# Kernel tuning notes

Measured on AMD Instinct MI355X. Metric: run time of the kernel, lower is better.

The kernel has to match this reference:

```python
import jax, jax.numpy as jnp
import numpy as np

N, E, B = 25000, 400000, 64          # nodes, edges, graphs
F, ED, H, C = 32, 8, 4, 32           # feature/edge dims, heads, per-head dim
HC = H * C
L = 4                                # init conv + 3 stacked convs (same shapes)
LIN = 128


def setup_inputs() -> dict:
    key = jax.random.key(0)
    ks = jax.random.split(key, 24)
    s = 0.05
    inp = {
        "x": jax.random.normal(ks[0], (N, F), jnp.float32),
        "edge_attr": jax.random.normal(ks[1], (E, ED), jnp.float32),
        "edge_index": jax.random.randint(ks[2], (2, E), 0, N),
        "batch_index": jnp.sort(jax.random.randint(ks[3], (N,), 0, B)),
        # stacked TransformerConv params (leading dim = layer)
        "Wq": jax.random.normal(ks[4], (L, F, HC), jnp.float32) * s,
        "bq": jnp.zeros((L, HC), jnp.float32),
        "Wk": jax.random.normal(ks[5], (L, F, HC), jnp.float32) * s,
        "bk": jnp.zeros((L, HC), jnp.float32),
        "Wv": jax.random.normal(ks[6], (L, F, HC), jnp.float32) * s,
        "bv": jnp.zeros((L, HC), jnp.float32),
        "We": jax.random.normal(ks[7], (L, ED, HC), jnp.float32) * s,
        "be": jnp.zeros((L, HC), jnp.float32),
        "Wskip": jax.random.normal(ks[8], (L, F, HC), jnp.float32) * s,
        "bskip": jnp.zeros((L, HC), jnp.float32),
        "Wbeta": jax.random.normal(ks[9], (L, 3 * HC, 1), jnp.float32) * s,
        # per-layer Linear(H*C -> emb) + BatchNorm
        "Wlin": jax.random.normal(ks[10], (L, HC, F), jnp.float32) * s,
        "blin": jnp.zeros((L, F), jnp.float32),
        "bn_gamma": jnp.ones((L, F), jnp.float32),
        "bn_beta": jnp.zeros((L, F), jnp.float32),
        # readout MLP
        "W1": jax.random.normal(ks[11], (2 * F, LIN), jnp.float32) * s,
        "b1": jnp.zeros((LIN,), jnp.float32),
        "W2": jax.random.normal(ks[12], (LIN, LIN // 2), jnp.float32) * s,
        "b2": jnp.zeros((LIN // 2,), jnp.float32),
        "W3": jax.random.normal(ks[13], (LIN // 2, 1), jnp.float32) * s,
        "b3": jnp.zeros((1,), jnp.float32),
    }
    return inp


def _transformer_conv(x, edge_attr, src, dst, Wq, bq, Wk, bk, Wv, bv, We, be,
                      Wskip, bskip, Wbeta):
    """PyG TransformerConv(heads=H, concat=True, beta=True, edge_dim=ED), eval mode."""
    n = x.shape[0]
    q = (x @ Wq + bq).reshape(n, H, C)
    k = (x @ Wk + bk).reshape(n, H, C)
    v = (x @ Wv + bv).reshape(n, H, C)
    e = (edge_attr @ We + be).reshape(-1, H, C)          # [E,H,C]
    kj = k[src] + e                                       # key_j + edge
    alpha = jnp.einsum('ehc,ehc->eh', q[dst], kj) / np.sqrt(C).astype(np.float32)
    # segment softmax over incoming edges per destination node
    amax = jax.ops.segment_max(alpha, dst, num_segments=n)
    a = jnp.exp(alpha - amax[dst])
    denom = jax.ops.segment_sum(a, dst, num_segments=n)
    a = a / denom[dst]                                    # [E,H]
    msg = (v[src] + e) * a[:, :, None]
    out = jax.ops.segment_sum(msg, dst, num_segments=n).reshape(n, HC)
    x_skip = x @ Wskip + bskip
    beta = jax.nn.sigmoid(
        jnp.concatenate([out, x_skip, out - x_skip], axis=-1) @ Wbeta)  # [N,1]
    return beta * x_skip + (1.0 - beta) * out


def _bn(h, gamma, beta):
    m = h.mean(axis=0)
    v = h.var(axis=0)
    return (h - m) * jax.lax.rsqrt(v + 1e-5) * gamma + beta


def reference(x, edge_attr, edge_index, batch_index,
              Wq, bq, Wk, bk, Wv, bv, We, be, Wskip, bskip, Wbeta,
              Wlin, blin, bn_gamma, bn_beta, W1, b1, W2, b2, W3, b3):
    src, dst = edge_index[0], edge_index[1]
    counts = jax.ops.segment_sum(jnp.ones((N,), jnp.float32), batch_index,
                                 num_segments=B)[:, None]
    h = x
    rep = jnp.zeros((B, 2 * F), jnp.float32)
    for i in range(L):
        h = _transformer_conv(h, edge_attr, src, dst,
                              Wq[i], bq[i], Wk[i], bk[i], Wv[i], bv[i],
                              We[i], be[i], Wskip[i], bskip[i], Wbeta[i])
        h = jax.nn.elu(h @ Wlin[i] + blin[i])
        h = _bn(h, bn_gamma[i], bn_beta[i])
        if i > 0:  # original pools only inside the n_layers loop
            gmx = jax.ops.segment_max(h, batch_index, num_segments=B)
            gmean = jax.ops.segment_sum(h, batch_index, num_segments=B) / counts
            rep = rep + jnp.concatenate([gmx, gmean], axis=1)
    z = jax.nn.elu(rep @ W1 + b1)
    z = jax.nn.elu(z @ W2 + b2)
    return z @ W3 + b3  # [B,1]
```

## Files before the change

kernel.cpp:

```cpp
#include <hip/hip_runtime.h>
#include <hip/hip_bf16.h>
#include <hip/hip_fp16.h>
#include <math.h>

#define NN 25000
#define EE 400000
#define BB 64
#define FF 32
#define EDD 8
#define HH 4
#define CC 32
#define HCC 128
#define LL 4
#define LINN 128

#define RSQRT_C 0.17677669529663687f
#define NREP 16
#define NREPP 8
#define GMAX_OFF (NREP * 64)
#define GSUM_OFF (NREP * 64 + NREPP * BB * 32)
#define LSTATS_WORDS (NREP * 64 + 2 * NREPP * BB * 32)


__global__ void deg_kernel(const int* __restrict__ dst, int* __restrict__ deg) {
    int i = blockIdx.x * blockDim.x + threadIdx.x;
    if (i < EE) atomicAdd(&deg[dst[i]], 1);
}

__global__ void scan1_kernel(const int* __restrict__ deg, int* __restrict__ rowp, int* __restrict__ blks) {
    __shared__ int s[256];
    int i = blockIdx.x * 256 + threadIdx.x;
    int v = (i < NN) ? deg[i] : 0;
    s[threadIdx.x] = v;
    __syncthreads();
    for (int off = 1; off < 256; off <<= 1) {
        int t = (threadIdx.x >= off) ? s[threadIdx.x - off] : 0;
        __syncthreads();
        s[threadIdx.x] += t;
        __syncthreads();
    }
    if (i < NN) rowp[i + 1] = s[threadIdx.x];
    if (threadIdx.x == 255) blks[blockIdx.x] = s[255];
    if (i == 0) rowp[0] = 0;
}

__global__ void scan2_kernel(int* __restrict__ blks, int nb,
                             const int* __restrict__ bidx, int* __restrict__ gstart) {
    __shared__ int s[128];
    int t = threadIdx.x;
    int v = (t < nb) ? blks[t] : 0;
    s[t] = v;
    __syncthreads();
    for (int off = 1; off < 128; off <<= 1) {
        int u = (t >= off) ? s[t - off] : 0;
        __syncthreads();
        s[t] += u;
        __syncthreads();
    }
    if (t < nb) blks[t] = s[t] - v;
    if (t <= BB) {
        int lo = 0, hi = NN;
        while (lo < hi) { int mid = (lo + hi) >> 1; if (bidx[mid] < t) lo = mid + 1; else hi = mid; }
        gstart[t] = lo;
    }
}

__global__ void scan3_kernel(int* __restrict__ rowp, const int* __restrict__ blks) {
    int i = blockIdx.x * 256 + threadIdx.x;
    if (i < NN) rowp[i + 1] += blks[blockIdx.x];
}

__global__ void fill_kernel(const int* __restrict__ dst, const int* __restrict__ rowp,
                            int* __restrict__ cnt2, int* __restrict__ eid) {
    int i = blockIdx.x * blockDim.x + threadIdx.x;
    if (i < EE) {
        int d = dst[i];
        int pos = rowp[d] + atomicAdd(&cnt2[d], 1);
        eid[pos] = i;
    }
}

__global__ void sortseg_kernel(const int* __restrict__ rowp, int* __restrict__ eid) {
    int n = blockIdx.x * 256 + threadIdx.x;
    if (n >= NN) return;
    int b = rowp[n], e = rowp[n + 1];
    int d = e - b;
    if (d <= 1) return;
    if (d <= 64) {
        int buf[64];
        for (int i = 0; i < d; ++i) buf[i] = eid[b + i];
        for (int i = 1; i < d; ++i) {
            int key = buf[i];
            int j = i - 1;
            while (j >= 0 && buf[j] > key) { buf[j + 1] = buf[j]; --j; }
            buf[j + 1] = key;
        }
        for (int i = 0; i < d; ++i) eid[b + i] = buf[i];
    } else {
        for (int i = b + 1; i < e; ++i) {
            int key = eid[i];
            int j = i - 1;
            while (j >= b && eid[j] > key) { eid[j + 1] = eid[j]; --j; }
            eid[j + 1] = key;
        }
    }
}

__global__ void csr_gather_kernel(const int* __restrict__ csre, const int* __restrict__ srcA,
                                  const float* __restrict__ eattr,
                                  int* __restrict__ csrsrc, uint4* __restrict__ eh) {
    int j = blockIdx.x * blockDim.x + threadIdx.x;
    if (j < EE) {
        int e = csre[j];
        csrsrc[j] = srcA[e];
        const float4* s = (const float4*)(eattr + (size_t)e * 8);
        float4 s0 = s[0], s1 = s[1];
        __half2 h0 = __float22half2_rn(make_float2(s0.x, s0.y));
        __half2 h1 = __float22half2_rn(make_float2(s0.z, s0.w));
        __half2 h2 = __float22half2_rn(make_float2(s1.x, s1.y));
        __half2 h3 = __float22half2_rn(make_float2(s1.z, s1.w));
        uint4 o;
        o.x = *(unsigned*)&h0; o.y = *(unsigned*)&h1;
        o.z = *(unsigned*)&h2; o.w = *(unsigned*)&h3;
        eh[j] = o;
    }
}

__global__ __launch_bounds__(256) void qkvs_kernel(
    const float* __restrict__ hin, int applyBN,
    const float* __restrict__ lstats_prev, float* __restrict__ lstats_cur,
    const float* __restrict__ gamma, const float* __restrict__ bnbeta,
    const float* __restrict__ Wq, const float* __restrict__ bq,
    const float* __restrict__ Wk, const float* __restrict__ bk,
    const float* __restrict__ Wv, const float* __restrict__ bv,
    const float* __restrict__ Ws, const float* __restrict__ bs,
    __half2* __restrict__ qo, __half2* __restrict__ kvo,
    __half2* __restrict__ so)
{
    if (blockIdx.x == 0) {
        for (int i = threadIdx.x; i < LSTATS_WORDS; i += 256) lstats_cur[i] = 0.0f;
    }
    __shared__ float xs[32][32];
    __shared__ float sbns[64];
    if (threadIdx.x < 32) {
        float scale = 1.0f, shift = 0.0f;
        if (applyBN) {
            float sm = 0.0f, sq = 0.0f;
#pragma unroll
            for (int r = 0; r < NREP; ++r) {
                sm += lstats_prev[r * 64 + threadIdx.x];
                sq += lstats_prev[r * 64 + 32 + threadIdx.x];
            }
            float mean = sm * (1.0f / NN);
            float var = sq * (1.0f / NN) - mean * mean;
            scale = gamma[threadIdx.x] * rsqrtf(var + 1e-5f);
            shift = bnbeta[threadIdx.x] - mean * scale;
        }
        sbns[threadIdx.x] = scale;
        sbns[32 + threadIdx.x] = shift;
    }
    int lane = threadIdx.x & 63;
    int sel = threadIdx.x >> 6;
    const float* W = (sel == 0) ? Wq : (sel == 1) ? Wk : (sel == 2) ? Wv : Ws;
    const float* bias = (sel == 0) ? bq : (sel == 1) ? bk : (sel == 2) ? bv : bs;
    float w0[32], w1[32];
#pragma unroll
    for (int f = 0; f < 32; ++f) {
        float2 t = *(const float2*)&W[f * 128 + 2 * lane];
        w0[f] = t.x; w1[f] = t.y;
    }
    float2 bvv = *(const float2*)&bias[2 * lane];

    int c = lane >> 1;
    int pr = lane & 1;
    int h2k = c * 4 + pr;
    int h2v = c * 4 + 2 + pr;

    for (int chunk = blockIdx.x * 32; chunk < NN; chunk += gridDim.x * 32) {
        __syncthreads();
        for (int i = threadIdx.x; i < 1024; i += 256) {
            int nn = chunk + (i >> 5);
            int ch = i & 31;
            float v = (nn < NN) ? hin[nn * 32 + ch] : 0.0f;
            xs[i >> 5][ch] = v * sbns[ch] + sbns[32 + ch];
        }
        __syncthreads();
        int nmax = NN - chunk; if (nmax > 32) nmax = 32;
        for (int nl = 0; nl < nmax; ++nl) {
            float a0 = bvv.x, a1 = bvv.y;
#pragma unroll
            for (int f4 = 0; f4 < 8; ++f4) {
                float4 xv = *(const float4*)&xs[nl][f4 * 4];
                a0 = fmaf(xv.x, w0[f4 * 4],     a0);
                a1 = fmaf(xv.x, w1[f4 * 4],     a1);
                a0 = fmaf(xv.y, w0[f4 * 4 + 1], a0);
                a1 = fmaf(xv.y, w1[f4 * 4 + 1], a1);
                a0 = fmaf(xv.z, w0[f4 * 4 + 2], a0);
                a1 = fmaf(xv.z, w1[f4 * 4 + 2], a1);
                a0 = fmaf(xv.w, w0[f4 * 4 + 3], a0);
                a1 = fmaf(xv.w, w1[f4 * 4 + 3], a1);
            }
            size_t node = (size_t)(chunk + nl);
            __half2 hv = __float22half2_rn(make_float2(a0, a1));
            if (sel == 0)      qo[node * 64 + lane] = hv;
            else if (sel == 1) kvo[node * 128 + h2k] = hv;
            else if (sel == 2) kvo[node * 128 + h2v] = hv;
            else               so[node * 64 + lane] = hv;
        }
    }
}

__device__ __forceinline__ unsigned fmap_u(float x) {
    unsigned u = __float_as_uint(x);
    return (u & 0x80000000u) ? ~u : (u | 0x80000000u);
}
__device__ __forceinline__ float funmap_u(unsigned u) {
    unsigned b = (u & 0x80000000u) ? (u & 0x7fffffffu) : ~u;
    return __uint_as_float(b);
}

__global__ __launch_bounds__(256) void attn_kernel(
    const uint2* __restrict__ qh, const uint4* __restrict__ kvb4,
    const uint2* __restrict__ skh,
    const uint4* __restrict__ eh,
    const int* __restrict__ srcArr,
    const int* __restrict__ rowp,
    const int* __restrict__ bidx,
    const float* __restrict__ WeL, const float* __restrict__ beL,
    const float* __restrict__ WbL,
    const float* __restrict__ WlinL, const float* __restrict__ blinL,
    float* __restrict__ hlin, float* __restrict__ lstats,
    int doPool, int doWriteH)
{
    __shared__ __align__(16) float shc[4 * 128];
    __shared__ float sbn[64];

    int tid = threadIdx.x;
    if (tid < 64) sbn[tid] = 0.0f;
    __syncthreads();

    int w = tid >> 6;
    int lane = tid & 63;
    int n = blockIdx.x * 4 + w;

    if (n < NN) {
        int c = lane & 31;
        int h = lane >> 5;

        float4 we[8];
#pragma unroll
        for (int d = 0; d < 8; ++d) we[d] = *(const float4*)&WeL[d * 128 + 4 * c];
        float4 be4 = *(const float4*)&beL[4 * c];

        uint2 qraw = qh[(size_t)n * 32 + c];
        float2 q01 = __half22float2(*(const __half2*)&qraw.x);
        float2 q23 = __half22float2(*(const __half2*)&qraw.y);
        float4 q4 = make_float4(q01.x * RSQRT_C, q01.y * RSQRT_C,
                                q23.x * RSQRT_C, q23.y * RSQRT_C);

        int beg = rowp[n], end = rowp[n + 1];
        int cnt = end - beg;
        int last = end - 1;

        float s = 0.0f, a0 = 0.0f, a1 = 0.0f, a2 = 0.0f, a3 = 0.0f;

        uint4 kvA = make_uint4(0u, 0u, 0u, 0u), kvB = kvA;
        uint4 eaA = kvA, eaB = kvA;
        int snC = 0, snD = 0;

        if (cnt > 0) {
            int j0 = beg + h;     j0 = (j0 < end) ? j0 : last;
            int j1 = beg + 2 + h; j1 = (j1 < end) ? j1 : last;
            int j2 = beg + 4 + h; j2 = (j2 < end) ? j2 : last;
            int j3 = beg + 6 + h; j3 = (j3 < end) ? j3 : last;
            int snA = srcArr[j0];
            int snB = srcArr[j1];
            snC = srcArr[j2];
            snD = srcArr[j3];
            kvA = kvb4[(size_t)snA * 32 + c];
            kvB = kvb4[(size_t)snB * 32 + c];
            eaA = eh[j0];
            eaB = eh[j1];
        }

        for (int jb = beg; jb < end; jb += 2) {
            int j = jb + h;
            uint4 kvC = kvb4[(size_t)snC * 32 + c];
            int jn = (j + 4 < end) ? j + 4 : last;
            uint4 eaC = eh[jn];
            int j8 = (j + 8 < end) ? j + 8 : last;
            int snE = srcArr[j8];

            float2 e01 = __half22float2(*(const __half2*)&eaA.x);
            float2 e23 = __half22float2(*(const __half2*)&eaA.y);
            float2 e45 = __half22float2(*(const __half2*)&eaA.z);
            float2 e67 = __half22float2(*(const __half2*)&eaA.w);
            float ead[8] = { e01.x, e01.y, e23.x, e23.y, e45.x, e45.y, e67.x, e67.y };

            float ex = be4.x, ey = be4.y, ez = be4.z, ew = be4.w;
#pragma unroll
            for (int d = 0; d < 8; ++d) {
                ex = fmaf(ead[d], we[d].x, ex);
                ey = fmaf(ead[d], we[d].y, ey);
                ez = fmaf(ead[d], we[d].z, ez);
                ew = fmaf(ead[d], we[d].w, ew);
            }

            float2 k01 = __half22float2(*(const __half2*)&kvA.x);
            float2 k23 = __half22float2(*(const __half2*)&kvA.y);
            float2 v01 = __half22float2(*(const __half2*)&kvA.z);
            float2 v23 = __half22float2(*(const __half2*)&kvA.w);

            float p = q4.x * (k01.x + ex) + q4.y * (k01.y + ey)
                    + q4.z * (k23.x + ez) + q4.w * (k23.y + ew);
            p += __shfl_xor(p, 1);
            p += __shfl_xor(p, 2);
            p += __shfl_xor(p, 4);
            float wg = (j < end) ? __expf(p) : 0.0f;
            s += wg;
            a0 = fmaf(wg, v01.x + ex, a0);
            a1 = fmaf(wg, v01.y + ey, a1);
            a2 = fmaf(wg, v23.x + ez, a2);
            a3 = fmaf(wg, v23.y + ew, a3);

            kvA = kvB; kvB = kvC;
            eaA = eaB; eaB = eaC;
            snC = snD; snD = snE;
        }

        s  += __shfl_xor(s, 32);
        a0 += __shfl_xor(a0, 32);
        a1 += __shfl_xor(a1, 32);
        a2 += __shfl_xor(a2, 32);
        a3 += __shfl_xor(a3, 32);

        float rs = (cnt > 0) ? (1.0f / s) : 0.0f;
        float o0 = a0 * rs, o1 = a1 * rs, o2 = a2 * rs, o3 = a3 * rs;

        uint2 skraw = skh[(size_t)n * 32 + c];
        float2 s01 = __half22float2(*(const __half2*)&skraw.x);
        float2 s23 = __half22float2(*(const __half2*)&skraw.y);
        float4 sk4 = make_float4(s01.x, s01.y, s23.x, s23.y);

        float4 wbo = *(const float4*)&WbL[4 * c];
        float4 wbs = *(const float4*)&WbL[128 + 4 * c];
        float4 wbd = *(const float4*)&WbL[256 + 4 * c];

        float t = o0 * wbo.x + sk4.x * wbs.x + (o0 - sk4.x) * wbd.x
                + o1 * wbo.y + sk4.y * wbs.y + (o1 - sk4.y) * wbd.y
                + o2 * wbo.z + sk4.z * wbs.z + (o2 - sk4.z) * wbd.z
                + o3 * wbo.w + sk4.w * wbs.w + (o3 - sk4.w) * wbd.w;
#pragma unroll
        for (int off = 1; off <= 16; off <<= 1) t += __shfl_xor(t, off);
        float beta = 1.0f / (1.0f + __expf(-t));
        float4 hc4;
        hc4.x = beta * sk4.x + (1.0f - beta) * o0;
        hc4.y = beta * sk4.y + (1.0f - beta) * o1;
        hc4.z = beta * sk4.z + (1.0f - beta) * o2;
        hc4.w = beta * sk4.w + (1.0f - beta) * o3;
        if (h == 0) ((float4*)shc)[w * 32 + c] = hc4;
        int cc = lane & 31;
        int half = lane >> 5;
        float acc = 0.0f;
#pragma unroll 8
        for (int i = 0; i < 64; ++i) {
            int ch = half * 64 + i;
            acc += shc[w * 128 + ch] * WlinL[ch * 32 + cc];
        }
        acc += __shfl_xor(acc, 32);
        if (lane < 32) {
            float hv = acc + blinL[lane];
            hv = (hv > 0.0f) ? hv : expm1f(hv);
            if (doWriteH) hlin[n * 32 + lane] = hv;
            atomicAdd(&sbn[lane], hv);
            atomicAdd(&sbn[32 + lane], hv * hv);
            if (doPool) {
                int g = bidx[n];
                int repv = blockIdx.x & (NREPP - 1);
                size_t idx = ((size_t)repv * BB + g) * 32 + lane;
                atomicMax((unsigned*)lstats + GMAX_OFF + idx, fmap_u(hv));
                atomicAdd(lstats + GSUM_OFF + idx, hv);
            }
        }
    }
    __syncthreads();
    if (tid < 64) atomicAdd(&lstats[(blockIdx.x & (NREP - 1)) * 64 + tid], sbn[tid]);
}

__global__ void repupd_kernel(const float* __restrict__ lstats,
                              const float* __restrict__ gamma, const float* __restrict__ bnbeta,
                              const int* __restrict__ gstart, float* __restrict__ rep, int assign) {
    int i = blockIdx.x * blockDim.x + threadIdx.x;
    if (i < BB * 32) {
        int g = i >> 5, ch = i & 31;
        float sm = 0.0f, sq = 0.0f;
#pragma unroll
        for (int r = 0; r < NREP; ++r) { sm += lstats[r * 64 + ch]; sq += lstats[r * 64 + 32 + ch]; }
        float mean = sm * (1.0f / NN);
        float var = sq * (1.0f / NN) - mean * mean;
        float scale = gamma[ch] * rsqrtf(var + 1e-5f);
        float shift = bnbeta[ch] - mean * scale;

        int cntg = gstart[g + 1] - gstart[g];
        float vmax = 0.0f, vmean = 0.0f;
        if (cntg > 0) {
            const unsigned* gm = (const unsigned*)lstats + GMAX_OFF;
            const float* gs = lstats + GSUM_OFF;
            unsigned mx = 0u;
            float sum = 0.0f;
#pragma unroll
            for (int r = 0; r < NREPP; ++r) {
                size_t idx = ((size_t)r * BB + g) * 32 + ch;
                unsigned m = gm[idx];
                mx = (m > mx) ? m : mx;
                sum += gs[idx];
            }
            vmax = scale * funmap_u(mx) + shift;
            vmean = scale * (sum / (float)cntg) + shift;
        }
        if (assign) {
            rep[g * 64 + ch] = vmax;
            rep[g * 64 + 32 + ch] = vmean;
        } else {
            rep[g * 64 + ch] += vmax;
            rep[g * 64 + 32 + ch] += vmean;
        }
    }
}

__device__ __forceinline__ float eluf(float x) { return x > 0.0f ? x : expm1f(x); }

__global__ __launch_bounds__(128) void readout_kernel(
    const float* __restrict__ rep,
    const float* __restrict__ W1, const float* __restrict__ b1,
    const float* __restrict__ W2, const float* __restrict__ b2,
    const float* __restrict__ W3, const float* __restrict__ b3,
    float* __restrict__ out)
{
    __shared__ float sr[64];
    __shared__ float sz1[128];
    __shared__ float sz2[64];
    int g = blockIdx.x;
    int t = threadIdx.x;
    if (t < 64) sr[t] = rep[g * 64 + t];
    __syncthreads();
    float acc = b1[t];
#pragma unroll 8
    for (int i = 0; i < 64; ++i) acc += sr[i] * W1[i * 128 + t];
    sz1[t] = eluf(acc);
    __syncthreads();
    if (t < 64) {
        float a2 = b2[t];
#pragma unroll 8
        for (int i = 0; i < 128; ++i) a2 += sz1[i] * W2[i * 64 + t];
        sz2[t] = eluf(a2);
    }
    __syncthreads();
    if (t < 64) {
        float p = sz2[t] * W3[t];
#pragma unroll
        for (int off = 1; off <= 32; off <<= 1) p += __shfl_xor(p, off);
        if (t == 0) out[g] = p + b3[0];
    }
}


extern "C" void kernel_launch(void* const* d_in, const int* in_sizes, int n_in,
                              void* d_out, int out_size, void* d_ws, size_t ws_size,
                              hipStream_t stream) {
    const float* x      = (const float*)d_in[0];
    const float* eattr  = (const float*)d_in[1];
    const int*   eidx   = (const int*)d_in[2];
    const int*   bidx   = (const int*)d_in[3];
    const float* Wq     = (const float*)d_in[4];
    const float* bq     = (const float*)d_in[5];
    const float* Wk     = (const float*)d_in[6];
    const float* bk     = (const float*)d_in[7];
    const float* Wv     = (const float*)d_in[8];
    const float* bv     = (const float*)d_in[9];
    const float* We     = (const float*)d_in[10];
    const float* be     = (const float*)d_in[11];
    const float* Wskip  = (const float*)d_in[12];
    const float* bskip  = (const float*)d_in[13];
    const float* Wbeta  = (const float*)d_in[14];
    const float* Wlin   = (const float*)d_in[15];
    const float* blin   = (const float*)d_in[16];
    const float* bng    = (const float*)d_in[17];
    const float* bnb    = (const float*)d_in[18];
    const float* W1     = (const float*)d_in[19];
    const float* b1     = (const float*)d_in[20];
    const float* W2     = (const float*)d_in[21];
    const float* b2     = (const float*)d_in[22];
    const float* W3     = (const float*)d_in[23];
    const float* b3     = (const float*)d_in[24];
    float* out = (float*)d_out;

    char* ws = (char*)d_ws;
    size_t off = 0;
    auto alloc = [&](size_t bytes) -> char* {
        char* p = ws + off;
        off = (off + bytes + 255) & ~(size_t)255;
        return p;
    };
    int*     rowp   = (int*)alloc((NN + 1) * 4);
    int*     degcnt = (int*)alloc(2 * NN * 4);
    int*     deg    = degcnt;
    int*     cnt2   = degcnt + NN;
    int*     csre   = (int*)alloc(EE * 4);
    int*     blks   = (int*)alloc(128 * 4);
    int*     gstart = (int*)alloc((BB + 1) * 4);
    float*   rep    = (float*)alloc(BB * 64 * 4);
    __half2* qH     = (__half2*)alloc((size_t)NN * 64 * 4);
    __half2* kvB    = (__half2*)alloc((size_t)NN * 128 * 4);
    __half2* skH    = (__half2*)alloc((size_t)NN * 64 * 4);
    float*   hlin   = (float*)alloc((size_t)NN * 32 * 4);
    float*   lstats = (float*)alloc(2 * LSTATS_WORDS * 4);
    int*     csrsrc = (int*)alloc(EE * 4);
    uint4*   ecsrh  = (uint4*)alloc((size_t)EE * 16);

    const int* srcA = eidx;
    const int* dstA = eidx + EE;

    (void)hipMemsetAsync(degcnt, 0, 2 * NN * 4, stream);

    deg_kernel<<<(EE + 255) / 256, 256, 0, stream>>>(dstA, deg);
    scan1_kernel<<<98, 256, 0, stream>>>(deg, rowp, blks);
    scan2_kernel<<<1, 128, 0, stream>>>(blks, 98, bidx, gstart);
    scan3_kernel<<<98, 256, 0, stream>>>(rowp, blks);
    fill_kernel<<<(EE + 255) / 256, 256, 0, stream>>>(dstA, rowp, cnt2, csre);
    sortseg_kernel<<<98, 256, 0, stream>>>(rowp, csre);
    csr_gather_kernel<<<(EE + 255) / 256, 256, 0, stream>>>(csre, srcA, eattr, csrsrc, ecsrh);

    for (int l = 0; l < LL; ++l) {
        float* lcur = lstats + (size_t)(l & 1) * LSTATS_WORDS;
        float* lprev = lstats + (size_t)((l & 1) ^ 1) * LSTATS_WORDS;

        qkvs_kernel<<<782, 256, 0, stream>>>(
            (l == 0) ? x : hlin, (l > 0) ? 1 : 0,
            lprev, lcur,
            bng + (l > 0 ? (l - 1) : 0) * FF, bnb + (l > 0 ? (l - 1) : 0) * FF,
            Wq + l * FF * HCC, bq + l * HCC,
            Wk + l * FF * HCC, bk + l * HCC,
            Wv + l * FF * HCC, bv + l * HCC,
            Wskip + l * FF * HCC, bskip + l * HCC,
            qH, kvB, skH);

        attn_kernel<<<(NN + 3) / 4, 256, 0, stream>>>(
            (const uint2*)qH, (const uint4*)kvB, (const uint2*)skH,
            ecsrh, csrsrc, rowp, bidx,
            We + l * EDD * HCC, be + l * HCC,
            Wbeta + l * 3 * HCC,
            Wlin + l * HCC * FF, blin + l * FF,
            hlin, lcur,
            (l > 0) ? 1 : 0, (l < LL - 1) ? 1 : 0);

        if (l > 0) {
            repupd_kernel<<<8, 256, 0, stream>>>(lcur, bng + l * FF, bnb + l * FF,
                                                 gstart, rep, (l == 1) ? 1 : 0);
        }
    }

    readout_kernel<<<64, 128, 0, stream>>>(rep, W1, b1, W2, b2, W3, b3, out);
}
```

Measured before the change: 532.3 us.

## Schedule attention nodes by descending degree and fold pooling update into readout

```diff
diff --git a/kernel.cpp b/kernel.cpp
--- a/kernel.cpp
+++ b/kernel.cpp
@@ -27,11 +27,13 @@
     if (i < EE) atomicAdd(&deg[dst[i]], 1);
 }
 
-__global__ void scan1_kernel(const int* __restrict__ deg, int* __restrict__ rowp, int* __restrict__ blks) {
+__global__ void scan1_kernel(const int* __restrict__ deg, int* __restrict__ rowp,
+                             int* __restrict__ blks, int* __restrict__ hist) {
     __shared__ int s[256];
     int i = blockIdx.x * 256 + threadIdx.x;
     int v = (i < NN) ? deg[i] : 0;
     s[threadIdx.x] = v;
+    if (i < NN) atomicAdd(&hist[v < 255 ? v : 255], 1);
     __syncthreads();
     for (int off = 1; off < 256; off <<= 1) {
         int t = (threadIdx.x >= off) ? s[threadIdx.x - off] : 0;
@@ -44,8 +46,27 @@
     if (i == 0) rowp[0] = 0;
 }
 
-__global__ void scan2_kernel(int* __restrict__ blks, int nb,
-                             const int* __restrict__ bidx, int* __restrict__ gstart) {
+__global__ void scan2_kernel(const int* __restrict__ bidx, int* __restrict__ gstart,
+                             const int* __restrict__ hist, int* __restrict__ binstart) {
+    __shared__ int sb[256];
+    int t = threadIdx.x;
+    sb[t] = hist[t];
+    __syncthreads();
+    for (int off = 1; off < 256; off <<= 1) {
+        int u = (t + off < 256) ? sb[t + off] : 0;
+        __syncthreads();
+        sb[t] += u;
+        __syncthreads();
+    }
+    binstart[t] = sb[t] - hist[t];
+    if (t <= BB) {
+        int lo = 0, hi = NN;
+        while (lo < hi) { int mid = (lo + hi) >> 1; if (bidx[mid] < t) lo = mid + 1; else hi = mid; }
+        gstart[t] = lo;
+    }
+}
+
+__global__ void scan2b_kernel(int* __restrict__ blks, int nb) {
     __shared__ int s[128];
     int t = threadIdx.x;
     int v = (t < nb) ? blks[t] : 0;
@@ -58,16 +79,18 @@
         __syncthreads();
     }
     if (t < nb) blks[t] = s[t] - v;
-    if (t <= BB) {
-        int lo = 0, hi = NN;
-        while (lo < hi) { int mid = (lo + hi) >> 1; if (bidx[mid] < t) lo = mid + 1; else hi = mid; }
-        gstart[t] = lo;
-    }
-}
-
-__global__ void scan3_kernel(int* __restrict__ rowp, const int* __restrict__ blks) {
+}
+
+__global__ void scan3_kernel(int* __restrict__ rowp, const int* __restrict__ blks,
+                             const int* __restrict__ deg, const int* __restrict__ binstart,
+                             int* __restrict__ bincnt, int* __restrict__ perm) {
     int i = blockIdx.x * 256 + threadIdx.x;
-    if (i < NN) rowp[i + 1] += blks[blockIdx.x];
+    if (i < NN) {
+        rowp[i + 1] += blks[blockIdx.x];
+        int d = deg[i]; d = (d < 255) ? d : 255;
+        int pos = binstart[d] + atomicAdd(&bincnt[d], 1);
+        perm[pos] = i;
+    }
 }
 
 __global__ void fill_kernel(const int* __restrict__ dst, const int* __restrict__ rowp,
@@ -226,6 +249,7 @@
     const int* __restrict__ srcArr,
     const int* __restrict__ rowp,
     const int* __restrict__ bidx,
+    const int* __restrict__ perm,
     const float* __restrict__ WeL, const float* __restrict__ beL,
     const float* __restrict__ WbL,
     const float* __restrict__ WlinL, const float* __restrict__ blinL,
@@ -234,16 +258,18 @@
 {
     __shared__ __align__(16) float shc[4 * 128];
     __shared__ float sbn[64];
+    __shared__ int snode[4];
 
     int tid = threadIdx.x;
     if (tid < 64) sbn[tid] = 0.0f;
+    if (tid < 4) snode[tid] = perm[blockIdx.x * 4 + tid];
     __syncthreads();
 
     int w = tid >> 6;
     int lane = tid & 63;
-    int n = blockIdx.x * 4 + w;
-
-    if (n < NN) {
+    int n = snode[w];
+
+    {
         int c = lane & 31;
         int h = lane >> 5;
 
@@ -387,51 +413,11 @@
     if (tid < 64) atomicAdd(&lstats[(blockIdx.x & (NREP - 1)) * 64 + tid], sbn[tid]);
 }
 
-__global__ void repupd_kernel(const float* __restrict__ lstats,
-                              const float* __restrict__ gamma, const float* __restrict__ bnbeta,
-                              const int* __restrict__ gstart, float* __restrict__ rep, int assign) {
-    int i = blockIdx.x * blockDim.x + threadIdx.x;
-    if (i < BB * 32) {
-        int g = i >> 5, ch = i & 31;
-        float sm = 0.0f, sq = 0.0f;
-#pragma unroll
-        for (int r = 0; r < NREP; ++r) { sm += lstats[r * 64 + ch]; sq += lstats[r * 64 + 32 + ch]; }
-        float mean = sm * (1.0f / NN);
-        float var = sq * (1.0f / NN) - mean * mean;
-        float scale = gamma[ch] * rsqrtf(var + 1e-5f);
-        float shift = bnbeta[ch] - mean * scale;
-
-        int cntg = gstart[g + 1] - gstart[g];
-        float vmax = 0.0f, vmean = 0.0f;
-        if (cntg > 0) {
-            const unsigned* gm = (const unsigned*)lstats + GMAX_OFF;
-            const float* gs = lstats + GSUM_OFF;
-            unsigned mx = 0u;
-            float sum = 0.0f;
-#pragma unroll
-            for (int r = 0; r < NREPP; ++r) {
-                size_t idx = ((size_t)r * BB + g) * 32 + ch;
-                unsigned m = gm[idx];
-                mx = (m > mx) ? m : mx;
-                sum += gs[idx];
-            }
-            vmax = scale * funmap_u(mx) + shift;
-            vmean = scale * (sum / (float)cntg) + shift;
-        }
-        if (assign) {
-            rep[g * 64 + ch] = vmax;
-            rep[g * 64 + 32 + ch] = vmean;
-        } else {
-            rep[g * 64 + ch] += vmax;
-            rep[g * 64 + 32 + ch] += vmean;
-        }
-    }
-}
-
 __device__ __forceinline__ float eluf(float x) { return x > 0.0f ? x : expm1f(x); }
 
 __global__ __launch_bounds__(128) void readout_kernel(
-    const float* __restrict__ rep,
+    const float* __restrict__ lstats, const int* __restrict__ gstart,
+    const float* __restrict__ bng, const float* __restrict__ bnb,
     const float* __restrict__ W1, const float* __restrict__ b1,
     const float* __restrict__ W2, const float* __restrict__ b2,
     const float* __restrict__ W3, const float* __restrict__ b3,
@@ -440,9 +426,41 @@
     __shared__ float sr[64];
     __shared__ float sz1[128];
     __shared__ float sz2[64];
+    __shared__ float sss[64];
     int g = blockIdx.x;
     int t = threadIdx.x;
-    if (t < 64) sr[t] = rep[g * 64 + t];
+    if (t < 64) sr[t] = 0.0f;
+    int cntg = gstart[g + 1] - gstart[g];
+    for (int l = 1; l < LL; ++l) {
+        const float* lst = lstats + (size_t)l * LSTATS_WORDS;
+        __syncthreads();
+        if (t < 32) {
+            float sm = 0.0f, sq = 0.0f;
+#pragma unroll
+            for (int r = 0; r < NREP; ++r) { sm += lst[r * 64 + t]; sq += lst[r * 64 + 32 + t]; }
+            float mean = sm * (1.0f / NN);
+            float var = sq * (1.0f / NN) - mean * mean;
+            float scale = bng[l * FF + t] * rsqrtf(var + 1e-5f);
+            sss[t] = scale;
+            sss[32 + t] = bnb[l * FF + t] - mean * scale;
+        }
+        __syncthreads();
+        if (t < 32 && cntg > 0) {
+            const unsigned* gm = (const unsigned*)lst + GMAX_OFF;
+            const float* gs = lst + GSUM_OFF;
+            unsigned mx = 0u;
+            float sum = 0.0f;
+#pragma unroll
+            for (int r = 0; r < NREPP; ++r) {
+                size_t idx = ((size_t)r * BB + g) * 32 + t;
+                unsigned m = gm[idx];
+                mx = (m > mx) ? m : mx;
+                sum += gs[idx];
+            }
+            sr[t]      += sss[t] * funmap_u(mx) + sss[32 + t];
+            sr[32 + t] += sss[t] * (sum / (float)cntg) + sss[32 + t];
+        }
+    }
     __syncthreads();
     float acc = b1[t];
 #pragma unroll 8
@@ -503,37 +521,41 @@
         return p;
     };
     int*     rowp   = (int*)alloc((NN + 1) * 4);
-    int*     degcnt = (int*)alloc(2 * NN * 4);
-    int*     deg    = degcnt;
-    int*     cnt2   = degcnt + NN;
+    int*     zeroed = (int*)alloc((2 * NN + 512) * 4);
+    int*     deg    = zeroed;
+    int*     cnt2   = zeroed + NN;
+    int*     hist   = zeroed + 2 * NN;
+    int*     bincnt = zeroed + 2 * NN + 256;
+    int*     binstart = (int*)alloc(256 * 4);
+    int*     perm   = (int*)alloc(NN * 4);
     int*     csre   = (int*)alloc(EE * 4);
     int*     blks   = (int*)alloc(128 * 4);
     int*     gstart = (int*)alloc((BB + 1) * 4);
-    float*   rep    = (float*)alloc(BB * 64 * 4);
     __half2* qH     = (__half2*)alloc((size_t)NN * 64 * 4);
     __half2* kvB    = (__half2*)alloc((size_t)NN * 128 * 4);
     __half2* skH    = (__half2*)alloc((size_t)NN * 64 * 4);
     float*   hlin   = (float*)alloc((size_t)NN * 32 * 4);
-    float*   lstats = (float*)alloc(2 * LSTATS_WORDS * 4);
+    float*   lstats = (float*)alloc((size_t)LL * LSTATS_WORDS * 4);
     int*     csrsrc = (int*)alloc(EE * 4);
     uint4*   ecsrh  = (uint4*)alloc((size_t)EE * 16);
 
     const int* srcA = eidx;
     const int* dstA = eidx + EE;
 
-    (void)hipMemsetAsync(degcnt, 0, 2 * NN * 4, stream);
+    (void)hipMemsetAsync(zeroed, 0, (2 * NN + 512) * 4, stream);
 
     deg_kernel<<<(EE + 255) / 256, 256, 0, stream>>>(dstA, deg);
-    scan1_kernel<<<98, 256, 0, stream>>>(deg, rowp, blks);
-    scan2_kernel<<<1, 128, 0, stream>>>(blks, 98, bidx, gstart);
-    scan3_kernel<<<98, 256, 0, stream>>>(rowp, blks);
+    scan1_kernel<<<98, 256, 0, stream>>>(deg, rowp, blks, hist);
+    scan2_kernel<<<1, 256, 0, stream>>>(bidx, gstart, hist, binstart);
+    scan2b_kernel<<<1, 128, 0, stream>>>(blks, 98);
+    scan3_kernel<<<98, 256, 0, stream>>>(rowp, blks, deg, binstart, bincnt, perm);
     fill_kernel<<<(EE + 255) / 256, 256, 0, stream>>>(dstA, rowp, cnt2, csre);
     sortseg_kernel<<<98, 256, 0, stream>>>(rowp, csre);
     csr_gather_kernel<<<(EE + 255) / 256, 256, 0, stream>>>(csre, srcA, eattr, csrsrc, ecsrh);
 
     for (int l = 0; l < LL; ++l) {
-        float* lcur = lstats + (size_t)(l & 1) * LSTATS_WORDS;
-        float* lprev = lstats + (size_t)((l & 1) ^ 1) * LSTATS_WORDS;
+        float* lcur = lstats + (size_t)l * LSTATS_WORDS;
+        float* lprev = lstats + (size_t)(l > 0 ? l - 1 : 0) * LSTATS_WORDS;
 
         qkvs_kernel<<<782, 256, 0, stream>>>(
             (l == 0) ? x : hlin, (l > 0) ? 1 : 0,
@@ -547,18 +569,14 @@
 
         attn_kernel<<<(NN + 3) / 4, 256, 0, stream>>>(
             (const uint2*)qH, (const uint4*)kvB, (const uint2*)skH,
-            ecsrh, csrsrc, rowp, bidx,
+            ecsrh, csrsrc, rowp, bidx, perm,
             We + l * EDD * HCC, be + l * HCC,
             Wbeta + l * 3 * HCC,
             Wlin + l * HCC * FF, blin + l * FF,
             hlin, lcur,
             (l > 0) ? 1 : 0, (l < LL - 1) ? 1 : 0);
-
-        if (l > 0) {
-            repupd_kernel<<<8, 256, 0, stream>>>(lcur, bng + l * FF, bnb + l * FF,
-                                                 gstart, rep, (l == 1) ? 1 : 0);
-        }
-    }
-
-    readout_kernel<<<64, 128, 0, stream>>>(rep, W1, b1, W2, b2, W3, b3, out);
-}
+    }
+
+    readout_kernel<<<64, 128, 0, stream>>>(lstats, gstart, bng, bnb,
+                                           W1, b1, W2, b2, W3, b3, out);
+}
```

Result: slower. 616.3 us (+15.8%).

## Order attention nodes by in-degree bins to balance warps per block

Applied to the files above, without the earlier changes.

```diff
diff --git a/kernel.cpp b/kernel.cpp
--- a/kernel.cpp
+++ b/kernel.cpp
@@ -27,11 +27,13 @@
     if (i < EE) atomicAdd(&deg[dst[i]], 1);
 }
 
-__global__ void scan1_kernel(const int* __restrict__ deg, int* __restrict__ rowp, int* __restrict__ blks) {
+__global__ void scan1_kernel(const int* __restrict__ deg, int* __restrict__ rowp,
+                             int* __restrict__ blks, int* __restrict__ hist) {
     __shared__ int s[256];
     int i = blockIdx.x * 256 + threadIdx.x;
     int v = (i < NN) ? deg[i] : 0;
     s[threadIdx.x] = v;
+    if (i < NN) atomicAdd(&hist[v < 255 ? v : 255], 1);
     __syncthreads();
     for (int off = 1; off < 256; off <<= 1) {
         int t = (threadIdx.x >= off) ? s[threadIdx.x - off] : 0;
@@ -65,9 +67,30 @@
     }
 }
 
-__global__ void scan3_kernel(int* __restrict__ rowp, const int* __restrict__ blks) {
+__global__ void binprep_kernel(const int* __restrict__ hist, int* __restrict__ binstart) {
+    __shared__ int sb[256];
+    int t = threadIdx.x;
+    sb[t] = hist[t];
+    __syncthreads();
+    for (int off = 1; off < 256; off <<= 1) {
+        int u = (t + off < 256) ? sb[t + off] : 0;
+        __syncthreads();
+        sb[t] += u;
+        __syncthreads();
+    }
+    binstart[t] = sb[t] - hist[t];
+}
+
+__global__ void scan3_kernel(int* __restrict__ rowp, const int* __restrict__ blks,
+                             const int* __restrict__ deg, const int* __restrict__ binstart,
+                             int* __restrict__ bincnt, int* __restrict__ perm) {
     int i = blockIdx.x * 256 + threadIdx.x;
-    if (i < NN) rowp[i + 1] += blks[blockIdx.x];
+    if (i < NN) {
+        rowp[i + 1] += blks[blockIdx.x];
+        int d = deg[i]; d = (d < 255) ? d : 255;
+        int pos = binstart[d] + atomicAdd(&bincnt[d], 1);
+        perm[pos] = i;
+    }
 }
 
 __global__ void fill_kernel(const int* __restrict__ dst, const int* __restrict__ rowp,
@@ -226,6 +249,7 @@
     const int* __restrict__ srcArr,
     const int* __restrict__ rowp,
     const int* __restrict__ bidx,
+    const int* __restrict__ perm,
     const float* __restrict__ WeL, const float* __restrict__ beL,
     const float* __restrict__ WbL,
     const float* __restrict__ WlinL, const float* __restrict__ blinL,
@@ -234,16 +258,18 @@
 {
     __shared__ __align__(16) float shc[4 * 128];
     __shared__ float sbn[64];
+    __shared__ int snode[4];
 
     int tid = threadIdx.x;
     if (tid < 64) sbn[tid] = 0.0f;
+    if (tid < 4) snode[tid] = perm[blockIdx.x * 4 + tid];
     __syncthreads();
 
     int w = tid >> 6;
     int lane = tid & 63;
-    int n = blockIdx.x * 4 + w;
-
-    if (n < NN) {
+    int n = snode[w];
+
+    {
         int c = lane & 31;
         int h = lane >> 5;
 
@@ -503,9 +529,13 @@
         return p;
     };
     int*     rowp   = (int*)alloc((NN + 1) * 4);
-    int*     degcnt = (int*)alloc(2 * NN * 4);
-    int*     deg    = degcnt;
-    int*     cnt2   = degcnt + NN;
+    int*     zeroed = (int*)alloc((2 * NN + 512) * 4);
+    int*     deg    = zeroed;
+    int*     cnt2   = zeroed + NN;
+    int*     hist   = zeroed + 2 * NN;
+    int*     bincnt = zeroed + 2 * NN + 256;
+    int*     binstart = (int*)alloc(256 * 4);
+    int*     perm   = (int*)alloc(NN * 4);
     int*     csre   = (int*)alloc(EE * 4);
     int*     blks   = (int*)alloc(128 * 4);
     int*     gstart = (int*)alloc((BB + 1) * 4);
@@ -521,12 +551,13 @@
     const int* srcA = eidx;
     const int* dstA = eidx + EE;
 
-    (void)hipMemsetAsync(degcnt, 0, 2 * NN * 4, stream);
+    (void)hipMemsetAsync(zeroed, 0, (2 * NN + 512) * 4, stream);
 
     deg_kernel<<<(EE + 255) / 256, 256, 0, stream>>>(dstA, deg);
-    scan1_kernel<<<98, 256, 0, stream>>>(deg, rowp, blks);
+    scan1_kernel<<<98, 256, 0, stream>>>(deg, rowp, blks, hist);
     scan2_kernel<<<1, 128, 0, stream>>>(blks, 98, bidx, gstart);
-    scan3_kernel<<<98, 256, 0, stream>>>(rowp, blks);
+    binprep_kernel<<<1, 256, 0, stream>>>(hist, binstart);
+    scan3_kernel<<<98, 256, 0, stream>>>(rowp, blks, deg, binstart, bincnt, perm);
     fill_kernel<<<(EE + 255) / 256, 256, 0, stream>>>(dstA, rowp, cnt2, csre);
     sortseg_kernel<<<98, 256, 0, stream>>>(rowp, csre);
     csr_gather_kernel<<<(EE + 255) / 256, 256, 0, stream>>>(csre, srcA, eattr, csrsrc, ecsrh);
@@ -545,9 +576,9 @@
             Wskip + l * FF * HCC, bskip + l * HCC,
             qH, kvB, skH);
 
-        attn_kernel<<<(NN + 3) / 4, 256, 0, stream>>>(
+        attn_kernel<<<NN / 4, 256, 0, stream>>>(
             (const uint2*)qH, (const uint4*)kvB, (const uint2*)skH,
-            ecsrh, csrsrc, rowp, bidx,
+            ecsrh, csrsrc, rowp, bidx, perm,
             We + l * EDD * HCC, be + l * HCC,
             Wbeta + l * 3 * HCC,
             Wlin + l * HCC * FF, blin + l * FF,
```

New measurement: 618.1 us. 16.1% more time.
